# Kernel tuning notes

Measured on AMD Instinct MI355X. Metric: run time of the kernel, lower is better.

## Reference

```python
import jax, jax.numpy as jnp
import numpy as np

B, T, D = 8, 4096, 1024


def setup_inputs() -> dict:
    key = jax.random.key(0)
    k1, k2 = jax.random.split(key)
    x = jax.random.normal(k1, (B, T, D), dtype=jnp.float32)
    lengths = jax.random.randint(k2, (B,), 0, T, dtype=jnp.int64)
    return {"x": x, "lengths": lengths}


def reference(x, lengths):
    # x: [B, T, D]; lengths: [B]
    # Original torch code materializes a [B,T,T,D] tensor via
    # (tril * pairwise_padding_mask)[..., None] * gelu(x)[:, None] and sums over
    # the source axis. Algebraically:
    #   out[b,i] = x[b,i] + m[b,i] * sum_{j<=i} m[b,j] * gelu(x[b,j])
    # where m[b,t] = (t < lengths[b]). This is a masked causal prefix sum.
    t = x.shape[1]
    valid = (jnp.arange(t)[None, :] < lengths[:, None]).astype(x.dtype)  # [B,T]
    g = jax.nn.gelu(x, approximate=False) * valid[:, :, None]           # [B,T,D]
    prefix = jnp.cumsum(g, axis=1)                                      # [B,T,D]
    return x + valid[:, :, None] * prefix
```

## Files before the change

### kernel.cpp

```cpp
#include <hip/hip_runtime.h>
#include <math.h>

#define BB 8
#define TT 4096
#define DD 1024
#define NC 256
#define CT (TT / NC)
#define D4 (DD / 4)

typedef float vfloat4 __attribute__((ext_vector_type(4)));

__device__ __forceinline__ float gelu_exact(float v) {
    return 0.5f * v * (1.0f + erff(v * 0.70710678118654752f));
}

__global__ __launch_bounds__(256)
void k_partial(const float* __restrict__ x, const int* __restrict__ lengths,
               float* __restrict__ ws) {
    const int c  = blockIdx.x;
    const int b  = blockIdx.y;
    const int d4 = threadIdx.x;
    const int len = lengths[b];
    const int t0 = c * CT;
    const int t1 = min(t0 + CT, len);

    const float4* __restrict__ xp = (const float4*)(x + (size_t)b * TT * DD);
    float4 s = make_float4(0.f, 0.f, 0.f, 0.f);
    #pragma unroll 4
    for (int t = t0; t < t1; ++t) {
        float4 v = xp[(size_t)t * D4 + d4];
        s.x += gelu_exact(v.x);
        s.y += gelu_exact(v.y);
        s.z += gelu_exact(v.z);
        s.w += gelu_exact(v.w);
    }
    ((float4*)ws)[((size_t)b * NC + c) * D4 + d4] = s;
}

__global__ __launch_bounds__(256)
void k_scan(float* __restrict__ ws) {
    const int b     = blockIdx.x >> 2;
    const int dtile = blockIdx.x & 3;
    const int d     = dtile * 256 + threadIdx.x;
    float* p = ws + (size_t)b * NC * DD + d;
    float run = 0.f;
    #pragma unroll 8
    for (int c = 0; c < NC; ++c) {
        float v = p[(size_t)c * DD];
        p[(size_t)c * DD] = run;
        run += v;
    }
}

__global__ __launch_bounds__(256)
void k_apply(const float* __restrict__ x, const int* __restrict__ lengths,
             const float* __restrict__ ws, float* __restrict__ out) {
    const int c  = blockIdx.x;
    const int b  = blockIdx.y;
    const int d4 = threadIdx.x;
    const int len = lengths[b];
    const int t0 = c * CT;
    const int tv = min(t0 + CT, len);

    const float4* __restrict__ xp = (const float4*)(x + (size_t)b * TT * DD);
    vfloat4* __restrict__ op = (vfloat4*)(out + (size_t)b * TT * DD);

    float4 pre = ((const float4*)ws)[((size_t)b * NC + c) * D4 + d4];

    int t = t0;
    #pragma unroll 4
    for (; t < tv; ++t) {
        float4 v = xp[(size_t)t * D4 + d4];
        pre.x += gelu_exact(v.x);
        pre.y += gelu_exact(v.y);
        pre.z += gelu_exact(v.z);
        pre.w += gelu_exact(v.w);
        vfloat4 o = {v.x + pre.x, v.y + pre.y, v.z + pre.z, v.w + pre.w};
        __builtin_nontemporal_store(o, &op[(size_t)t * D4 + d4]);
    }
    #pragma unroll 4
    for (; t < t0 + CT; ++t) {
        float4 v = xp[(size_t)t * D4 + d4];
        vfloat4 o = {v.x, v.y, v.z, v.w};
        __builtin_nontemporal_store(o, &op[(size_t)t * D4 + d4]);
    }
}

extern "C" void kernel_launch(void* const* d_in, const int* in_sizes, int n_in,
                              void* d_out, int out_size, void* d_ws, size_t ws_size,
                              hipStream_t stream) {
    const float* x       = (const float*)d_in[0];
    const int*   lengths = (const int*)d_in[1];
    float*       out     = (float*)d_out;
    float*       ws      = (float*)d_ws;

    dim3 blk(256, 1, 1);
    dim3 g1(NC, BB, 1);
    hipLaunchKernelGGL(k_partial, g1, blk, 0, stream, x, lengths, ws);

    dim3 g2(BB * 4, 1, 1);
    hipLaunchKernelGGL(k_scan, g2, blk, 0, stream, ws);

    hipLaunchKernelGGL(k_apply, g1, blk, 0, stream, x, lengths, ws, out);
}
```

Measured before the change: 267.7 us.

## Fuse partial, scan and apply into one cooperative kernel with grid sync

Replaces the three-kernel partial/scan/apply pipeline with one cooperative kernel. Each block reduces its chunk, writes the aggregate, waits at a grid-wide barrier, then sums the preceding chunk aggregates and applies the prefix. This removes two kernel launches and the serial scan kernel. The cost is far fewer blocks (512 instead of 2048, with longer chunks), which lowers parallelism and load balance, plus grid-sync overhead. If the cooperative launch fails, the old three-kernel path runs instead.

```diff
diff --git a/kernel.cpp b/kernel.cpp
--- a/kernel.cpp
+++ b/kernel.cpp
@@ -1,17 +1,81 @@
 #include <hip/hip_runtime.h>
+#include <hip/hip_cooperative_groups.h>
 #include <math.h>
+
+namespace cg = cooperative_groups;
 
 #define BB 8
 #define TT 4096
 #define DD 1024
-#define NC 256
-#define CT (TT / NC)
 #define D4 (DD / 4)
+
+#define NCC 64
+#define CTC (TT / NCC)
+
+#define NCF 256
+#define CTF (TT / NCF)
 
 typedef float vfloat4 __attribute__((ext_vector_type(4)));
 
 __device__ __forceinline__ float gelu_exact(float v) {
     return 0.5f * v * (1.0f + erff(v * 0.70710678118654752f));
+}
+
+__device__ __forceinline__ void gelu_acc(float4& s, const float4 v) {
+    s.x += gelu_exact(v.x);
+    s.y += gelu_exact(v.y);
+    s.z += gelu_exact(v.z);
+    s.w += gelu_exact(v.w);
+}
+
+__global__ __launch_bounds__(256, 2)
+void k_fused(const float* __restrict__ x, const int* __restrict__ lengths,
+             float* __restrict__ ws, float* __restrict__ out) {
+    const int c  = blockIdx.x;
+    const int b  = blockIdx.y;
+    const int d4 = threadIdx.x;
+    const int len = lengths[b];
+    const int t0 = c * CTC;
+    const int tv = min(t0 + CTC, len);
+
+    const float4* __restrict__ xp = (const float4*)(x + (size_t)b * TT * DD);
+
+    float4 s = make_float4(0.f, 0.f, 0.f, 0.f);
+    #pragma unroll 4
+    for (int t = t0; t < tv; ++t) {
+        float4 v = xp[(size_t)t * D4 + d4];
+        gelu_acc(s, v);
+    }
+    float4* aggw = (float4*)ws + ((size_t)b * NCC + c) * D4 + d4;
+    *aggw = s;
+
+    __threadfence();
+    cg::this_grid().sync();
+    __threadfence();
+
+    float4 pre = make_float4(0.f, 0.f, 0.f, 0.f);
+    const float4* aggp = (const float4*)ws + (size_t)b * NCC * D4 + d4;
+    #pragma unroll 8
+    for (int cc = 0; cc < c; ++cc) {
+        float4 a = aggp[(size_t)cc * D4];
+        pre.x += a.x; pre.y += a.y; pre.z += a.z; pre.w += a.w;
+    }
+
+    vfloat4* __restrict__ op = (vfloat4*)(out + (size_t)b * TT * DD);
+    int t = t0;
+    #pragma unroll 4
+    for (; t < tv; ++t) {
+        float4 v = xp[(size_t)t * D4 + d4];
+        gelu_acc(pre, v);
+        vfloat4 o = {v.x + pre.x, v.y + pre.y, v.z + pre.z, v.w + pre.w};
+        __builtin_nontemporal_store(o, &op[(size_t)t * D4 + d4]);
+    }
+    #pragma unroll 4
+    for (; t < t0 + CTC; ++t) {
+        float4 v = xp[(size_t)t * D4 + d4];
+        vfloat4 o = {v.x, v.y, v.z, v.w};
+        __builtin_nontemporal_store(o, &op[(size_t)t * D4 + d4]);
+    }
 }
 
 __global__ __launch_bounds__(256)
@@ -21,20 +85,17 @@
     const int b  = blockIdx.y;
     const int d4 = threadIdx.x;
     const int len = lengths[b];
-    const int t0 = c * CT;
-    const int t1 = min(t0 + CT, len);
+    const int t0 = c * CTF;
+    const int t1 = min(t0 + CTF, len);
 
     const float4* __restrict__ xp = (const float4*)(x + (size_t)b * TT * DD);
     float4 s = make_float4(0.f, 0.f, 0.f, 0.f);
     #pragma unroll 4
     for (int t = t0; t < t1; ++t) {
         float4 v = xp[(size_t)t * D4 + d4];
-        s.x += gelu_exact(v.x);
-        s.y += gelu_exact(v.y);
-        s.z += gelu_exact(v.z);
-        s.w += gelu_exact(v.w);
+        gelu_acc(s, v);
     }
-    ((float4*)ws)[((size_t)b * NC + c) * D4 + d4] = s;
+    ((float4*)ws)[((size_t)b * NCF + c) * D4 + d4] = s;
 }
 
 __global__ __launch_bounds__(256)
@@ -42,10 +103,10 @@
     const int b     = blockIdx.x >> 2;
     const int dtile = blockIdx.x & 3;
     const int d     = dtile * 256 + threadIdx.x;
-    float* p = ws + (size_t)b * NC * DD + d;
+    float* p = ws + (size_t)b * NCF * DD + d;
     float run = 0.f;
     #pragma unroll 8
-    for (int c = 0; c < NC; ++c) {
+    for (int c = 0; c < NCF; ++c) {
         float v = p[(size_t)c * DD];
         p[(size_t)c * DD] = run;
         run += v;
@@ -59,27 +120,24 @@
     const int b  = blockIdx.y;
     const int d4 = threadIdx.x;
     const int len = lengths[b];
-    const int t0 = c * CT;
-    const int tv = min(t0 + CT, len);
+    const int t0 = c * CTF;
+    const int tv = min(t0 + CTF, len);
 
     const float4* __restrict__ xp = (const float4*)(x + (size_t)b * TT * DD);
     vfloat4* __restrict__ op = (vfloat4*)(out + (size_t)b * TT * DD);
 
-    float4 pre = ((const float4*)ws)[((size_t)b * NC + c) * D4 + d4];
+    float4 pre = ((const float4*)ws)[((size_t)b * NCF + c) * D4 + d4];
 
     int t = t0;
     #pragma unroll 4
     for (; t < tv; ++t) {
         float4 v = xp[(size_t)t * D4 + d4];
-        pre.x += gelu_exact(v.x);
-        pre.y += gelu_exact(v.y);
-        pre.z += gelu_exact(v.z);
-        pre.w += gelu_exact(v.w);
+        gelu_acc(pre, v);
         vfloat4 o = {v.x + pre.x, v.y + pre.y, v.z + pre.z, v.w + pre.w};
         __builtin_nontemporal_store(o, &op[(size_t)t * D4 + d4]);
     }
     #pragma unroll 4
-    for (; t < t0 + CT; ++t) {
+    for (; t < t0 + CTF; ++t) {
         float4 v = xp[(size_t)t * D4 + d4];
         vfloat4 o = {v.x, v.y, v.z, v.w};
         __builtin_nontemporal_store(o, &op[(size_t)t * D4 + d4]);
@@ -95,11 +153,16 @@
     float*       ws      = (float*)d_ws;
 
     dim3 blk(256, 1, 1);
-    dim3 g1(NC, BB, 1);
-    hipLaunchKernelGGL(k_partial, g1, blk, 0, stream, x, lengths, ws);
+    dim3 grd(NCC, BB, 1);
 
-    dim3 g2(BB * 4, 1, 1);
-    hipLaunchKernelGGL(k_scan, g2, blk, 0, stream, ws);
-
-    hipLaunchKernelGGL(k_apply, g1, blk, 0, stream, x, lengths, ws, out);
+    void* args[] = {(void*)&x, (void*)&lengths, (void*)&ws, (void*)&out};
+    hipError_t err = hipLaunchCooperativeKernel((void*)k_fused, grd, blk,
+                                                args, 0, stream);
+    if (err != hipSuccess) {
+        dim3 g1(NCF, BB, 1);
+        hipLaunchKernelGGL(k_partial, g1, blk, 0, stream, x, lengths, ws);
+        dim3 g2(BB * 4, 1, 1);
+        hipLaunchKernelGGL(k_scan, g2, blk, 0, stream, ws);
+        hipLaunchKernelGGL(k_apply, g1, blk, 0, stream, x, lengths, ws, out);
+    }
 }
```

Measured after the change: 453.4 us. 1.69x slower.

## Drop separate scan kernel; each apply block sums preceding chunk aggregates

Applied to the files above, without the earlier changes.

Removes the serial k_scan kernel, which ran on only 32 blocks and walked 256 chunks sequentially. Each k_apply block now sums the raw per-chunk partials of all earlier chunks itself, using two accumulators. k_partial also returns early for chunks that lie entirely past the sequence length, skipping their workspace writes. This saves a launch and a low-parallelism pass, but adds O(c) redundant reads of the workspace per block (up to 255 float4 loads per thread for late chunks).

```diff
diff --git a/kernel.cpp b/kernel.cpp
--- a/kernel.cpp
+++ b/kernel.cpp
@@ -14,6 +14,13 @@
     return 0.5f * v * (1.0f + erff(v * 0.70710678118654752f));
 }
 
+__device__ __forceinline__ void gelu_acc(float4& s, const float4 v) {
+    s.x += gelu_exact(v.x);
+    s.y += gelu_exact(v.y);
+    s.z += gelu_exact(v.z);
+    s.w += gelu_exact(v.w);
+}
+
 __global__ __launch_bounds__(256)
 void k_partial(const float* __restrict__ x, const int* __restrict__ lengths,
                float* __restrict__ ws) {
@@ -22,6 +29,7 @@
     const int d4 = threadIdx.x;
     const int len = lengths[b];
     const int t0 = c * CT;
+    if (t0 >= len) return;
     const int t1 = min(t0 + CT, len);
 
     const float4* __restrict__ xp = (const float4*)(x + (size_t)b * TT * DD);
@@ -29,27 +37,9 @@
     #pragma unroll 4
     for (int t = t0; t < t1; ++t) {
         float4 v = xp[(size_t)t * D4 + d4];
-        s.x += gelu_exact(v.x);
-        s.y += gelu_exact(v.y);
-        s.z += gelu_exact(v.z);
-        s.w += gelu_exact(v.w);
+        gelu_acc(s, v);
     }
     ((float4*)ws)[((size_t)b * NC + c) * D4 + d4] = s;
-}
-
-__global__ __launch_bounds__(256)
-void k_scan(float* __restrict__ ws) {
-    const int b     = blockIdx.x >> 2;
-    const int dtile = blockIdx.x & 3;
-    const int d     = dtile * 256 + threadIdx.x;
-    float* p = ws + (size_t)b * NC * DD + d;
-    float run = 0.f;
-    #pragma unroll 8
-    for (int c = 0; c < NC; ++c) {
-        float v = p[(size_t)c * DD];
-        p[(size_t)c * DD] = run;
-        run += v;
-    }
 }
 
 __global__ __launch_bounds__(256)
@@ -65,18 +55,34 @@
     const float4* __restrict__ xp = (const float4*)(x + (size_t)b * TT * DD);
     vfloat4* __restrict__ op = (vfloat4*)(out + (size_t)b * TT * DD);
 
-    float4 pre = ((const float4*)ws)[((size_t)b * NC + c) * D4 + d4];
+    int t = t0;
+    if (t0 < len) {
+        float4 p0 = make_float4(0.f, 0.f, 0.f, 0.f);
+        float4 p1 = make_float4(0.f, 0.f, 0.f, 0.f);
+        const float4* __restrict__ aggp =
+            (const float4*)ws + (size_t)b * NC * D4 + d4;
+        int cc = 0;
+        #pragma unroll 4
+        for (; cc + 1 < c; cc += 2) {
+            float4 a0 = aggp[(size_t)cc * D4];
+            float4 a1 = aggp[(size_t)(cc + 1) * D4];
+            p0.x += a0.x; p0.y += a0.y; p0.z += a0.z; p0.w += a0.w;
+            p1.x += a1.x; p1.y += a1.y; p1.z += a1.z; p1.w += a1.w;
+        }
+        if (cc < c) {
+            float4 a0 = aggp[(size_t)cc * D4];
+            p0.x += a0.x; p0.y += a0.y; p0.z += a0.z; p0.w += a0.w;
+        }
+        float4 pre = make_float4(p0.x + p1.x, p0.y + p1.y,
+                                 p0.z + p1.z, p0.w + p1.w);
 
-    int t = t0;
-    #pragma unroll 4
-    for (; t < tv; ++t) {
-        float4 v = xp[(size_t)t * D4 + d4];
-        pre.x += gelu_exact(v.x);
-        pre.y += gelu_exact(v.y);
-        pre.z += gelu_exact(v.z);
-        pre.w += gelu_exact(v.w);
-        vfloat4 o = {v.x + pre.x, v.y + pre.y, v.z + pre.z, v.w + pre.w};
-        __builtin_nontemporal_store(o, &op[(size_t)t * D4 + d4]);
+        #pragma unroll 4
+        for (; t < tv; ++t) {
+            float4 v = xp[(size_t)t * D4 + d4];
+            gelu_acc(pre, v);
+            vfloat4 o = {v.x + pre.x, v.y + pre.y, v.z + pre.z, v.w + pre.w};
+            __builtin_nontemporal_store(o, &op[(size_t)t * D4 + d4]);
+        }
     }
     #pragma unroll 4
     for (; t < t0 + CT; ++t) {
@@ -97,9 +103,5 @@
     dim3 blk(256, 1, 1);
     dim3 g1(NC, BB, 1);
     hipLaunchKernelGGL(k_partial, g1, blk, 0, stream, x, lengths, ws);
-
-    dim3 g2(BB * 4, 1, 1);
-    hipLaunchKernelGGL(k_scan, g2, blk, 0, stream, ws);
-
-    hipLaunchKernelGGL(k_apply, g1, blk, 0, stream, x, lengths, ws, out);
+    hipLaunchKernelGGL(k_apply,   g1, blk, 0, stream, x, lengths, ws, out);
 }
```

Result: no change. 267.2 us (-0.2%).
